# Optimization experiments

Hardware: AMD Instinct MI355X
Metric: run time of the kernel (lower is better)

Reference implementation:

```python
import jax, jax.numpy as jnp
import numpy as np

SCALE = 20.0
EPS = 1e-8  # matches torch F.cosine_similarity eps


def _l2_normalize(x):
    # torch cosine_similarity clamps norms at eps
    norm = jnp.maximum(jnp.linalg.norm(x, axis=-1, keepdims=True), EPS)
    return x / norm


def setup_inputs() -> dict:
    key = jax.random.key(0)
    k1, k2 = jax.random.split(key)
    B, D = 4096, 1024
    anchor_emb = jax.random.normal(k1, (B, D), dtype=jnp.float32)
    pos_negs_emb = jax.random.normal(k2, (B, D), dtype=jnp.float32)
    return {"anchor_emb": anchor_emb, "pos_negs_emb": pos_negs_emb}


def reference(anchor_emb, pos_negs_emb):
    # cosine similarity as normalized GEMM (avoids (B,N,D) broadcast intermediate)
    a = _l2_normalize(anchor_emb)            # [B, D]
    p = _l2_normalize(pos_negs_emb)          # [N, D]
    scores = SCALE * jnp.einsum("bd,nd->bn", a, p)  # [B, N]
    B = scores.shape[0]
    # cross entropy with labels = arange(B): mean(logsumexp - diag)
    logZ = jax.scipy.special.logsumexp(scores, axis=1)  # [B]
    diag = scores[jnp.arange(B), jnp.arange(B)]          # [B]
    return jnp.mean(logZ - diag)
```

## Files before the change

kernel.cpp:

```cpp
#include <hip/hip_runtime.h>
#include <math.h>

#define NB 4096
#define ND 1024
#define SCALEF 20.0f

typedef __bf16 bf16_t;
typedef bf16_t bf16x4 __attribute__((ext_vector_type(4)));
typedef bf16_t bf16x8 __attribute__((ext_vector_type(8)));
typedef float floatx4 __attribute__((ext_vector_type(4)));

__device__ __forceinline__ void load16_to_lds(const void* g, void* l) {
    __builtin_amdgcn_global_load_lds(
        (const __attribute__((address_space(1))) void*)g,
        (__attribute__((address_space(3))) void*)l, 16, 0, 0);
}

__global__ __launch_bounds__(256) void mnrl_norm_cvt(
    const float* __restrict__ A, const float* __restrict__ P,
    bf16_t* __restrict__ Abf, bf16_t* __restrict__ Pbf,
    float* __restrict__ rowsum, float* __restrict__ out) {
    if (blockIdx.x == 0 && threadIdx.x == 0) out[0] = 0.0f;
    int row = blockIdx.x * 4 + (threadIdx.x >> 6);
    int lane = threadIdx.x & 63;
    bool is_a = row < NB;
    const float* src = is_a ? (A + (size_t)row * ND)
                            : (P + (size_t)(row - NB) * ND);
    bf16_t* dst = is_a ? (Abf + (size_t)row * ND)
                       : (Pbf + (size_t)(row - NB) * ND);

    float4 v[4];
    float ss = 0.0f;
#pragma unroll
    for (int i = 0; i < 4; ++i) {
        v[i] = ((const float4*)src)[i * 64 + lane];
        ss += v[i].x * v[i].x + v[i].y * v[i].y + v[i].z * v[i].z + v[i].w * v[i].w;
    }
#pragma unroll
    for (int off = 32; off > 0; off >>= 1) ss += __shfl_xor(ss, off, 64);
    float inv = 1.0f / fmaxf(sqrtf(ss), 1e-8f);
#pragma unroll
    for (int i = 0; i < 4; ++i) {
        bf16x4 w;
        w[0] = (bf16_t)(v[i].x * inv);
        w[1] = (bf16_t)(v[i].y * inv);
        w[2] = (bf16_t)(v[i].z * inv);
        w[3] = (bf16_t)(v[i].w * inv);
        ((bf16x4*)dst)[i * 64 + lane] = w;
    }
    if (is_a && lane == 0) rowsum[row] = 0.0f;
}

__global__ __launch_bounds__(512, 2) void mnrl_gemm_lse(
    const bf16_t* __restrict__ Abf, const bf16_t* __restrict__ Pbf,
    float* __restrict__ rowsum, float* __restrict__ diag) {
    __shared__ __align__(16) bf16_t lds_a[4][256 * 32];
    __shared__ __align__(16) bf16_t lds_b[4][256 * 32];

    int bid = blockIdx.x;
    int swz = (bid & 7) * 32 + (bid >> 3);
    int tile_m = swz >> 4;
    int tile_n = swz & 15;

    int t = threadIdx.x;
    int lane = t & 63;
    int w = t >> 6;
    int wm = w >> 2;
    int wn = w & 3;
    int quad = lane >> 4, l16 = lane & 15;

    const bf16_t* Abase = Abf + (size_t)tile_m * 256 * ND;
    const bf16_t* Pbase = Pbf + (size_t)tile_n * 256 * ND;

    int srow = lane >> 2;
    int chunk = (lane & 3) ^ ((lane >> 3) & 3);
    const bf16_t* srcA0 = Abase + (size_t)(w * 32 + srow) * ND + chunk * 8;
    const bf16_t* srcA1 = srcA0 + (size_t)16 * ND;
    const bf16_t* srcP0 = Pbase + (size_t)(w * 32 + srow) * ND + chunk * 8;
    const bf16_t* srcP1 = srcP0 + (size_t)16 * ND;
    const int dst0 = w * 1024;
    const int dst1 = w * 1024 + 512;

    int key = (l16 >> 1) & 3;
    int slot8 = (quad ^ key) * 8;
    int offA[8], offB[4];
#pragma unroll
    for (int mt = 0; mt < 8; ++mt)
        offA[mt] = (wm * 128 + mt * 16 + l16) * 32 + slot8;
#pragma unroll
    for (int nt = 0; nt < 4; ++nt)
        offB[nt] = (wn * 64 + nt * 16 + l16) * 32 + slot8;

    floatx4 acc[8][4];
#pragma unroll
    for (int mt = 0; mt < 8; ++mt)
#pragma unroll
        for (int nt = 0; nt < 4; ++nt) acc[mt][nt] = (floatx4){0.f, 0.f, 0.f, 0.f};

#define STAGE(KT)                                                   \
    {                                                               \
        int koff_ = (KT) * 32;                                      \
        int b_ = (KT) & 3;                                          \
        load16_to_lds(srcA0 + koff_, &lds_a[b_][dst0]);             \
        load16_to_lds(srcA1 + koff_, &lds_a[b_][dst1]);             \
        load16_to_lds(srcP0 + koff_, &lds_b[b_][dst0]);             \
        load16_to_lds(srcP1 + koff_, &lds_b[b_][dst1]);             \
    }

#define K_BODY(KT, DOSTAGE)                                                  \
    {                                                                        \
        int b_ = (KT) & 3;                                                   \
        if (DOSTAGE) STAGE((KT) + 3);                                        \
        bf16x8 af[8], bv[4];                                                 \
        _Pragma("unroll") for (int mt = 0; mt < 8; ++mt)                     \
            af[mt] = *(const bf16x8*)&lds_a[b_][offA[mt]];                   \
        _Pragma("unroll") for (int nt = 0; nt < 4; ++nt)                     \
            bv[nt] = *(const bf16x8*)&lds_b[b_][offB[nt]];                   \
        __builtin_amdgcn_s_setprio(1);                                       \
        _Pragma("unroll") for (int mt = 0; mt < 8; ++mt)                     \
            _Pragma("unroll") for (int nt = 0; nt < 4; ++nt)                 \
                acc[mt][nt] = __builtin_amdgcn_mfma_f32_16x16x32_bf16(       \
                    af[mt], bv[nt], acc[mt][nt], 0, 0, 0);                   \
        __builtin_amdgcn_s_setprio(0);                                       \
    }

    STAGE(0);
    STAGE(1);
    STAGE(2);

    for (int kt = 0; kt < 29; ++kt) {
        asm volatile("s_waitcnt vmcnt(8)" ::: "memory");
        __builtin_amdgcn_s_barrier();
        asm volatile("" ::: "memory");
        K_BODY(kt, 1);
    }
    asm volatile("s_waitcnt vmcnt(8)" ::: "memory");
    __builtin_amdgcn_s_barrier();
    asm volatile("" ::: "memory");
    K_BODY(29, 0);
    asm volatile("s_waitcnt vmcnt(4)" ::: "memory");
    __builtin_amdgcn_s_barrier();
    asm volatile("" ::: "memory");
    K_BODY(30, 0);
    asm volatile("s_waitcnt vmcnt(0)" ::: "memory");
    __builtin_amdgcn_s_barrier();
    asm volatile("" ::: "memory");
    K_BODY(31, 0);

#undef K_BODY
#undef STAGE

    bool diag_block = (tile_m == tile_n);
    float psum[8][4];
#pragma unroll
    for (int mt = 0; mt < 8; ++mt)
#pragma unroll
        for (int r = 0; r < 4; ++r) psum[mt][r] = 0.0f;

#pragma unroll
    for (int mt = 0; mt < 8; ++mt)
#pragma unroll
        for (int nt = 0; nt < 4; ++nt)
#pragma unroll
            for (int r = 0; r < 4; ++r) {
                float sc = SCALEF * acc[mt][nt][r];
                psum[mt][r] += __expf(sc - SCALEF);
                if (diag_block) {
                    int rt = wm * 128 + mt * 16 + quad * 4 + r;
                    int ct = wn * 64 + nt * 16 + l16;
                    if (rt == ct) diag[tile_m * 256 + rt] = sc;
                }
            }

    float* part = (float*)&lds_a[0][0];
#pragma unroll
    for (int mt = 0; mt < 8; ++mt)
#pragma unroll
        for (int r = 0; r < 4; ++r) {
            float v = psum[mt][r];
            v += __shfl_xor(v, 1, 64);
            v += __shfl_xor(v, 2, 64);
            v += __shfl_xor(v, 4, 64);
            v += __shfl_xor(v, 8, 64);
            if (l16 == 0) part[wn * 256 + wm * 128 + mt * 16 + quad * 4 + r] = v;
        }
    __syncthreads();
    if (t < 256) {
        float s = part[t] + part[256 + t] + part[512 + t] + part[768 + t];
        atomicAdd(&rowsum[tile_m * 256 + t], s);
    }
}

__global__ __launch_bounds__(256) void mnrl_finalize(const float* __restrict__ rowsum,
                                                     const float* __restrict__ diag,
                                                     float* __restrict__ out) {
    int t = threadIdx.x;
    int i = blockIdx.x * 256 + t;
    float local = (logf(rowsum[i]) + SCALEF) - diag[i];
#pragma unroll
    for (int off = 32; off > 0; off >>= 1) local += __shfl_down(local, off, 64);
    __shared__ float sred[4];
    if ((t & 63) == 0) sred[t >> 6] = local;
    __syncthreads();
    if (t == 0)
        atomicAdd(out, (sred[0] + sred[1] + sred[2] + sred[3]) * (1.0f / (float)NB));
}

extern "C" void kernel_launch(void* const* d_in, const int* in_sizes, int n_in,
                              void* d_out, int out_size, void* d_ws, size_t ws_size,
                              hipStream_t stream) {
    const float* A = (const float*)d_in[0];
    const float* P = (const float*)d_in[1];

    bf16_t* Abf = (bf16_t*)d_ws;
    bf16_t* Pbf = Abf + (size_t)NB * ND;
    float* rowsum = (float*)(Pbf + (size_t)NB * ND);
    float* diag = rowsum + NB;

    mnrl_norm_cvt<<<2 * NB / 4, 256, 0, stream>>>(A, P, Abf, Pbf, rowsum,
                                                  (float*)d_out);
    mnrl_gemm_lse<<<16 * 16, 512, 0, stream>>>(Abf, Pbf, rowsum, diag);
    mnrl_finalize<<<16, 256, 0, stream>>>(rowsum, diag, (float*)d_out);
}
```

Baseline: 122.0 us.

## Fuse normalize, GEMM-LSE and finalize into one cooperative kernel with grid syncs

Merges the three kernels (normalize+bf16 convert, GEMM with logsumexp partials, final reduction) into a single cooperative launch of 256 blocks, separated by grid-wide syncs. Each block normalizes 32 rows before the GEMM phase and reduces 16 rows afterwards. This removes two kernel launches and the gaps between them. In exchange it adds two grid barriers, and the normalize phase now runs on only 256 blocks of 512 threads instead of 2048 small blocks, which may lower memory parallelism in that phase.

```diff
diff --git a/kernel.cpp b/kernel.cpp
--- a/kernel.cpp
+++ b/kernel.cpp
@@ -1,5 +1,8 @@
 #include <hip/hip_runtime.h>
+#include <hip/hip_cooperative_groups.h>
 #include <math.h>
+
+namespace cg = cooperative_groups;
 
 #define NB 4096
 #define ND 1024
@@ -16,55 +19,59 @@
         (__attribute__((address_space(3))) void*)l, 16, 0, 0);
 }
 
-__global__ __launch_bounds__(256) void mnrl_norm_cvt(
+__global__ __launch_bounds__(512, 2) void mnrl_fused(
     const float* __restrict__ A, const float* __restrict__ P,
     bf16_t* __restrict__ Abf, bf16_t* __restrict__ Pbf,
-    float* __restrict__ rowsum, float* __restrict__ out) {
-    if (blockIdx.x == 0 && threadIdx.x == 0) out[0] = 0.0f;
-    int row = blockIdx.x * 4 + (threadIdx.x >> 6);
-    int lane = threadIdx.x & 63;
-    bool is_a = row < NB;
-    const float* src = is_a ? (A + (size_t)row * ND)
-                            : (P + (size_t)(row - NB) * ND);
-    bf16_t* dst = is_a ? (Abf + (size_t)row * ND)
-                       : (Pbf + (size_t)(row - NB) * ND);
-
-    float4 v[4];
-    float ss = 0.0f;
-#pragma unroll
-    for (int i = 0; i < 4; ++i) {
-        v[i] = ((const float4*)src)[i * 64 + lane];
-        ss += v[i].x * v[i].x + v[i].y * v[i].y + v[i].z * v[i].z + v[i].w * v[i].w;
-    }
-#pragma unroll
-    for (int off = 32; off > 0; off >>= 1) ss += __shfl_xor(ss, off, 64);
-    float inv = 1.0f / fmaxf(sqrtf(ss), 1e-8f);
-#pragma unroll
-    for (int i = 0; i < 4; ++i) {
-        bf16x4 w;
-        w[0] = (bf16_t)(v[i].x * inv);
-        w[1] = (bf16_t)(v[i].y * inv);
-        w[2] = (bf16_t)(v[i].z * inv);
-        w[3] = (bf16_t)(v[i].w * inv);
-        ((bf16x4*)dst)[i * 64 + lane] = w;
-    }
-    if (is_a && lane == 0) rowsum[row] = 0.0f;
-}
-
-__global__ __launch_bounds__(512, 2) void mnrl_gemm_lse(
-    const bf16_t* __restrict__ Abf, const bf16_t* __restrict__ Pbf,
-    float* __restrict__ rowsum, float* __restrict__ diag) {
+    float* __restrict__ rowsum, float* __restrict__ diag,
+    float* __restrict__ out) {
     __shared__ __align__(16) bf16_t lds_a[4][256 * 32];
     __shared__ __align__(16) bf16_t lds_b[4][256 * 32];
+
+    cg::grid_group grid = cg::this_grid();
+
+    int t = threadIdx.x;
+    int lane = t & 63;
+    int w = t >> 6;
+
+    if (blockIdx.x == 0 && t == 0) out[0] = 0.0f;
+    if (t < 16) rowsum[blockIdx.x * 16 + t] = 0.0f;
+#pragma unroll
+    for (int rr = 0; rr < 4; ++rr) {
+        int row = blockIdx.x * 32 + w * 4 + rr;
+        bool is_a = row < NB;
+        const float* src = is_a ? (A + (size_t)row * ND)
+                                : (P + (size_t)(row - NB) * ND);
+        bf16_t* dst = is_a ? (Abf + (size_t)row * ND)
+                           : (Pbf + (size_t)(row - NB) * ND);
+        float4 v[4];
+        float ss = 0.0f;
+#pragma unroll
+        for (int i = 0; i < 4; ++i) {
+            v[i] = ((const float4*)src)[i * 64 + lane];
+            ss += v[i].x * v[i].x + v[i].y * v[i].y + v[i].z * v[i].z +
+                  v[i].w * v[i].w;
+        }
+#pragma unroll
+        for (int off = 32; off > 0; off >>= 1) ss += __shfl_xor(ss, off, 64);
+        float inv = 1.0f / fmaxf(sqrtf(ss), 1e-8f);
+#pragma unroll
+        for (int i = 0; i < 4; ++i) {
+            bf16x4 wv;
+            wv[0] = (bf16_t)(v[i].x * inv);
+            wv[1] = (bf16_t)(v[i].y * inv);
+            wv[2] = (bf16_t)(v[i].z * inv);
+            wv[3] = (bf16_t)(v[i].w * inv);
+            ((bf16x4*)dst)[i * 64 + lane] = wv;
+        }
+    }
+
+    grid.sync();
 
     int bid = blockIdx.x;
     int swz = (bid & 7) * 32 + (bid >> 3);
     int tile_m = swz >> 4;
     int tile_n = swz & 15;
 
-    int t = threadIdx.x;
-    int lane = t & 63;
-    int w = t >> 6;
     int wm = w >> 2;
     int wn = w & 3;
     int quad = lane >> 4, l16 = lane & 15;
@@ -189,21 +196,22 @@
         float s = part[t] + part[256 + t] + part[512 + t] + part[768 + t];
         atomicAdd(&rowsum[tile_m * 256 + t], s);
     }
-}
-
-__global__ __launch_bounds__(256) void mnrl_finalize(const float* __restrict__ rowsum,
-                                                     const float* __restrict__ diag,
-                                                     float* __restrict__ out) {
-    int t = threadIdx.x;
-    int i = blockIdx.x * 256 + t;
-    float local = (logf(rowsum[i]) + SCALEF) - diag[i];
-#pragma unroll
-    for (int off = 32; off > 0; off >>= 1) local += __shfl_down(local, off, 64);
-    __shared__ float sred[4];
-    if ((t & 63) == 0) sred[t >> 6] = local;
-    __syncthreads();
-    if (t == 0)
-        atomicAdd(out, (sred[0] + sred[1] + sred[2] + sred[3]) * (1.0f / (float)NB));
+
+    grid.sync();
+
+    if (t < 16) {
+        int i = blockIdx.x * 16 + t;
+        float rs = __hip_atomic_load(&rowsum[i], __ATOMIC_RELAXED,
+                                     __HIP_MEMORY_SCOPE_AGENT);
+        float dg = __hip_atomic_load(&diag[i], __ATOMIC_RELAXED,
+                                     __HIP_MEMORY_SCOPE_AGENT);
+        float local = (logf(rs) + SCALEF) - dg;
+        local += __shfl_xor(local, 1, 64);
+        local += __shfl_xor(local, 2, 64);
+        local += __shfl_xor(local, 4, 64);
+        local += __shfl_xor(local, 8, 64);
+        if (t == 0) atomicAdd(out, local * (1.0f / (float)NB));
+    }
 }
 
 extern "C" void kernel_launch(void* const* d_in, const int* in_sizes, int n_in,
@@ -216,9 +224,10 @@
     bf16_t* Pbf = Abf + (size_t)NB * ND;
     float* rowsum = (float*)(Pbf + (size_t)NB * ND);
     float* diag = rowsum + NB;
-
-    mnrl_norm_cvt<<<2 * NB / 4, 256, 0, stream>>>(A, P, Abf, Pbf, rowsum,
-                                                  (float*)d_out);
-    mnrl_gemm_lse<<<16 * 16, 512, 0, stream>>>(Abf, Pbf, rowsum, diag);
-    mnrl_finalize<<<16, 256, 0, stream>>>(rowsum, diag, (float*)d_out);
+    float* out = (float*)d_out;
+
+    void* args[] = {(void*)&A,      (void*)&P,    (void*)&Abf, (void*)&Pbf,
+                    (void*)&rowsum, (void*)&diag, (void*)&out};
+    hipLaunchCooperativeKernel((const void*)mnrl_fused, dim3(256), dim3(512),
+                               args, 0, stream);
 }
```

After: 195.7 us. 1.6x slower.

## Quantize normalized embeddings to FP8 and use scaled f8f6f4 MFMA GEMM

Applied to the files above, without the earlier changes.

The normalize-and-convert kernel now writes each unit vector, multiplied by 16, as FP8 e4m3 instead of bf16, which halves workspace bytes. The GEMM uses the MI355X 16x16x128 scaled f8f6f4 MFMA with unit scales and rescales the result by 20/256 in the epilogue. The K loop shrinks to 8 steps of 128 with double buffering and a new XOR-swizzled LDS layout, replacing the 4-stage pipeline. This aims to double MFMA throughput and cut memory traffic, but FP8 quantization error enters scores multiplied by 20, which could affect accuracy, and the shallower pipeline waits on vmcnt(0) every step.

```diff
diff --git a/kernel.cpp b/kernel.cpp
--- a/kernel.cpp
+++ b/kernel.cpp
@@ -6,9 +6,9 @@
 #define SCALEF 20.0f
 
 typedef __bf16 bf16_t;
-typedef bf16_t bf16x4 __attribute__((ext_vector_type(4)));
-typedef bf16_t bf16x8 __attribute__((ext_vector_type(8)));
 typedef float floatx4 __attribute__((ext_vector_type(4)));
+typedef int intx4 __attribute__((ext_vector_type(4)));
+typedef int intx8 __attribute__((ext_vector_type(8)));
 
 __device__ __forceinline__ void load16_to_lds(const void* g, void* l) {
     __builtin_amdgcn_global_load_lds(
@@ -16,9 +16,19 @@
         (__attribute__((address_space(3))) void*)l, 16, 0, 0);
 }
 
+__device__ __forceinline__ intx8 ldfrag(const unsigned char* p0,
+                                        const unsigned char* p1) {
+    intx4 lo = *(const intx4*)p0;
+    intx4 hi = *(const intx4*)p1;
+    intx8 r;
+    r[0] = lo[0]; r[1] = lo[1]; r[2] = lo[2]; r[3] = lo[3];
+    r[4] = hi[0]; r[5] = hi[1]; r[6] = hi[2]; r[7] = hi[3];
+    return r;
+}
+
 __global__ __launch_bounds__(256) void mnrl_norm_cvt(
     const float* __restrict__ A, const float* __restrict__ P,
-    bf16_t* __restrict__ Abf, bf16_t* __restrict__ Pbf,
+    unsigned char* __restrict__ Afp, unsigned char* __restrict__ Pfp,
     float* __restrict__ rowsum, float* __restrict__ out) {
     if (blockIdx.x == 0 && threadIdx.x == 0) out[0] = 0.0f;
     int row = blockIdx.x * 4 + (threadIdx.x >> 6);
@@ -26,8 +36,8 @@
     bool is_a = row < NB;
     const float* src = is_a ? (A + (size_t)row * ND)
                             : (P + (size_t)(row - NB) * ND);
-    bf16_t* dst = is_a ? (Abf + (size_t)row * ND)
-                       : (Pbf + (size_t)(row - NB) * ND);
+    unsigned int* dst = (unsigned int*)(is_a ? (Afp + (size_t)row * ND)
+                                             : (Pfp + (size_t)(row - NB) * ND));
 
     float4 v[4];
     float ss = 0.0f;
@@ -38,24 +48,21 @@
     }
 #pragma unroll
     for (int off = 32; off > 0; off >>= 1) ss += __shfl_xor(ss, off, 64);
-    float inv = 1.0f / fmaxf(sqrtf(ss), 1e-8f);
+    float inv = 16.0f / fmaxf(sqrtf(ss), 1e-8f);
 #pragma unroll
     for (int i = 0; i < 4; ++i) {
-        bf16x4 w;
-        w[0] = (bf16_t)(v[i].x * inv);
-        w[1] = (bf16_t)(v[i].y * inv);
-        w[2] = (bf16_t)(v[i].z * inv);
-        w[3] = (bf16_t)(v[i].w * inv);
-        ((bf16x4*)dst)[i * 64 + lane] = w;
+        int pk = __builtin_amdgcn_cvt_pk_fp8_f32(v[i].x * inv, v[i].y * inv, 0, false);
+        pk = __builtin_amdgcn_cvt_pk_fp8_f32(v[i].z * inv, v[i].w * inv, pk, true);
+        dst[i * 64 + lane] = (unsigned int)pk;
     }
     if (is_a && lane == 0) rowsum[row] = 0.0f;
 }
 
 __global__ __launch_bounds__(512, 2) void mnrl_gemm_lse(
-    const bf16_t* __restrict__ Abf, const bf16_t* __restrict__ Pbf,
+    const unsigned char* __restrict__ Afp, const unsigned char* __restrict__ Pfp,
     float* __restrict__ rowsum, float* __restrict__ diag) {
-    __shared__ __align__(16) bf16_t lds_a[4][256 * 32];
-    __shared__ __align__(16) bf16_t lds_b[4][256 * 32];
+    __shared__ __align__(16) unsigned char lds_a[2][256 * 128];
+    __shared__ __align__(16) unsigned char lds_b[2][256 * 128];
 
     int bid = blockIdx.x;
     int swz = (bid & 7) * 32 + (bid >> 3);
@@ -67,29 +74,23 @@
     int w = t >> 6;
     int wm = w >> 2;
     int wn = w & 3;
-    int quad = lane >> 4, l16 = lane & 15;
-
-    const bf16_t* Abase = Abf + (size_t)tile_m * 256 * ND;
-    const bf16_t* Pbase = Pbf + (size_t)tile_n * 256 * ND;
-
-    int srow = lane >> 2;
-    int chunk = (lane & 3) ^ ((lane >> 3) & 3);
-    const bf16_t* srcA0 = Abase + (size_t)(w * 32 + srow) * ND + chunk * 8;
-    const bf16_t* srcA1 = srcA0 + (size_t)16 * ND;
-    const bf16_t* srcP0 = Pbase + (size_t)(w * 32 + srow) * ND + chunk * 8;
-    const bf16_t* srcP1 = srcP0 + (size_t)16 * ND;
-    const int dst0 = w * 1024;
-    const int dst1 = w * 1024 + 512;
-
-    int key = (l16 >> 1) & 3;
-    int slot8 = (quad ^ key) * 8;
-    int offA[8], offB[4];
-#pragma unroll
-    for (int mt = 0; mt < 8; ++mt)
-        offA[mt] = (wm * 128 + mt * 16 + l16) * 32 + slot8;
-#pragma unroll
-    for (int nt = 0; nt < 4; ++nt)
-        offB[nt] = (wn * 64 + nt * 16 + l16) * 32 + slot8;
+    int quad = lane >> 4;
+    int l16 = lane & 15;
+
+    const unsigned char* Abase = Afp + (size_t)tile_m * 256 * ND;
+    const unsigned char* Pbase = Pfp + (size_t)tile_n * 256 * ND;
+
+    int srow = lane >> 3;
+    int schunk = (lane & 7) ^ srow;
+    const unsigned char* sA = Abase + (size_t)(w * 32 + srow) * ND + schunk * 16;
+    const unsigned char* sP = Pbase + (size_t)(w * 32 + srow) * ND + schunk * 16;
+    const int sdst = w * 4096;
+
+    int e7 = l16 & 7;
+    int aoff0 = (wm * 128 + l16) * 128 + (((quad * 2 + 0) ^ e7) * 16);
+    int aoff1 = (wm * 128 + l16) * 128 + (((quad * 2 + 1) ^ e7) * 16);
+    int boff0 = (wn * 64 + l16) * 128 + (((quad * 2 + 0) ^ e7) * 16);
+    int boff1 = (wn * 64 + l16) * 128 + (((quad * 2 + 1) ^ e7) * 16);
 
     floatx4 acc[8][4];
 #pragma unroll
@@ -97,59 +98,48 @@
 #pragma unroll
         for (int nt = 0; nt < 4; ++nt) acc[mt][nt] = (floatx4){0.f, 0.f, 0.f, 0.f};
 
-#define STAGE(KT)                                                   \
-    {                                                               \
-        int koff_ = (KT) * 32;                                      \
-        int b_ = (KT) & 3;                                          \
-        load16_to_lds(srcA0 + koff_, &lds_a[b_][dst0]);             \
-        load16_to_lds(srcA1 + koff_, &lds_a[b_][dst1]);             \
-        load16_to_lds(srcP0 + koff_, &lds_b[b_][dst0]);             \
-        load16_to_lds(srcP1 + koff_, &lds_b[b_][dst1]);             \
-    }
-
-#define K_BODY(KT, DOSTAGE)                                                  \
+#define STAGE(KT)                                                            \
     {                                                                        \
-        int b_ = (KT) & 3;                                                   \
-        if (DOSTAGE) STAGE((KT) + 3);                                        \
-        bf16x8 af[8], bv[4];                                                 \
-        _Pragma("unroll") for (int mt = 0; mt < 8; ++mt)                     \
-            af[mt] = *(const bf16x8*)&lds_a[b_][offA[mt]];                   \
-        _Pragma("unroll") for (int nt = 0; nt < 4; ++nt)                     \
-            bv[nt] = *(const bf16x8*)&lds_b[b_][offB[nt]];                   \
-        __builtin_amdgcn_s_setprio(1);                                       \
-        _Pragma("unroll") for (int mt = 0; mt < 8; ++mt)                     \
-            _Pragma("unroll") for (int nt = 0; nt < 4; ++nt)                 \
-                acc[mt][nt] = __builtin_amdgcn_mfma_f32_16x16x32_bf16(       \
-                    af[mt], bv[nt], acc[mt][nt], 0, 0, 0);                   \
-        __builtin_amdgcn_s_setprio(0);                                       \
+        int ko_ = (KT) * 128;                                                \
+        int b_ = (KT) & 1;                                                   \
+        _Pragma("unroll") for (int j = 0; j < 4; ++j) {                      \
+            load16_to_lds(sA + (size_t)j * 8 * ND + ko_,                     \
+                          &lds_a[b_][sdst + j * 1024]);                      \
+            load16_to_lds(sP + (size_t)j * 8 * ND + ko_,                     \
+                          &lds_b[b_][sdst + j * 1024]);                      \
+        }                                                                    \
     }
 
     STAGE(0);
-    STAGE(1);
-    STAGE(2);
-
-    for (int kt = 0; kt < 29; ++kt) {
-        asm volatile("s_waitcnt vmcnt(8)" ::: "memory");
+
+    for (int kt = 0; kt < 8; ++kt) {
+        asm volatile("s_waitcnt vmcnt(0)" ::: "memory");
         __builtin_amdgcn_s_barrier();
         asm volatile("" ::: "memory");
-        K_BODY(kt, 1);
-    }
-    asm volatile("s_waitcnt vmcnt(8)" ::: "memory");
-    __builtin_amdgcn_s_barrier();
-    asm volatile("" ::: "memory");
-    K_BODY(29, 0);
-    asm volatile("s_waitcnt vmcnt(4)" ::: "memory");
-    __builtin_amdgcn_s_barrier();
-    asm volatile("" ::: "memory");
-    K_BODY(30, 0);
-    asm volatile("s_waitcnt vmcnt(0)" ::: "memory");
-    __builtin_amdgcn_s_barrier();
-    asm volatile("" ::: "memory");
-    K_BODY(31, 0);
-
-#undef K_BODY
+        if (kt < 7) STAGE(kt + 1);
+        const unsigned char* ba = &lds_a[kt & 1][0];
+        const unsigned char* bb = &lds_b[kt & 1][0];
+        intx8 bv[4];
+#pragma unroll
+        for (int nt = 0; nt < 4; ++nt)
+            bv[nt] = ldfrag(bb + boff0 + nt * 2048, bb + boff1 + nt * 2048);
+#pragma unroll
+        for (int mt = 0; mt < 8; ++mt) {
+            intx8 av = ldfrag(ba + aoff0 + mt * 2048, ba + aoff1 + mt * 2048);
+            __builtin_amdgcn_s_setprio(1);
+#pragma unroll
+            for (int nt = 0; nt < 4; ++nt)
+                acc[mt][nt] = __builtin_amdgcn_mfma_scale_f32_16x16x128_f8f6f4(
+                    av, bv[nt], acc[mt][nt],
+                    0 , 0 ,
+                    0, 0x7F7F7F7F ,
+                    0, 0x7F7F7F7F );
+            __builtin_amdgcn_s_setprio(0);
+        }
+    }
 #undef STAGE
 
+    const float SC = SCALEF / 256.0f;
     bool diag_block = (tile_m == tile_n);
     float psum[8][4];
 #pragma unroll
@@ -163,7 +153,7 @@
         for (int nt = 0; nt < 4; ++nt)
 #pragma unroll
             for (int r = 0; r < 4; ++r) {
-                float sc = SCALEF * acc[mt][nt][r];
+                float sc = SC * acc[mt][nt][r];
                 psum[mt][r] += __expf(sc - SCALEF);
                 if (diag_block) {
                     int rt = wm * 128 + mt * 16 + quad * 4 + r;
@@ -212,13 +202,13 @@
     const float* A = (const float*)d_in[0];
     const float* P = (const float*)d_in[1];
 
-    bf16_t* Abf = (bf16_t*)d_ws;
-    bf16_t* Pbf = Abf + (size_t)NB * ND;
-    float* rowsum = (float*)(Pbf + (size_t)NB * ND);
+    unsigned char* Afp = (unsigned char*)d_ws;
+    unsigned char* Pfp = Afp + (size_t)NB * ND;
+    float* rowsum = (float*)(Pfp + (size_t)NB * ND);
     float* diag = rowsum + NB;
 
-    mnrl_norm_cvt<<<2 * NB / 4, 256, 0, stream>>>(A, P, Abf, Pbf, rowsum,
+    mnrl_norm_cvt<<<2 * NB / 4, 256, 0, stream>>>(A, P, Afp, Pfp, rowsum,
                                                   (float*)d_out);
-    mnrl_gemm_lse<<<16 * 16, 512, 0, stream>>>(Abf, Pbf, rowsum, diag);
+    mnrl_gemm_lse<<<16 * 16, 512, 0, stream>>>(Afp, Pfp, rowsum, diag);
     mnrl_finalize<<<16, 256, 0, stream>>>(rowsum, diag, (float*)d_out);
 }
```

Measured after the change: 336.7 us. 2.76x slower.
